# Optimization experiments

Hardware: AMD Instinct MI355X
Metric: run time of the kernel (lower is better)

## Reference

```python
import jax, jax.numpy as jnp
import numpy as np
import math

B, S, F, H, E = 2, 1024, 512, 2048, 8
EPS = 1e-10

def setup_inputs() -> dict:
    key = jax.random.key(0)
    ks = jax.random.split(key, 6)
    s1 = math.sqrt(1.0 / (F + H))  # complex_xavier_init std for F->H
    s2 = math.sqrt(1.0 / (H + F))  # std for H->F
    return {
        'x_r': jax.random.normal(ks[0], (B, S, F), jnp.float32),
        'x_i': jax.random.normal(ks[1], (B, S, F), jnp.float32),
        'Wr1': jax.random.normal(ks[2], (E, F, H), jnp.float32) * s1,
        'Wi1': jax.random.normal(ks[3], (E, F, H), jnp.float32) * s1,
        'br1': jnp.zeros((E, H), jnp.float32),
        'bi1': jnp.zeros((E, H), jnp.float32),
        'mb': jnp.zeros((E, H), jnp.float32),  # ModReLU bias
        'Wr2': jax.random.normal(ks[4], (E, H, F), jnp.float32) * s2,
        'Wi2': jax.random.normal(ks[5], (E, H, F), jnp.float32) * s2,
        'br2': jnp.zeros((E, F), jnp.float32),
        'bi2': jnp.zeros((E, F), jnp.float32),
    }

def reference(x_r, x_i, Wr1, Wi1, br1, bi1, mb, Wr2, Wi2, br2, bi2):
    n_exp = Wr1.shape[0]
    # --- PhaseRouter: deterministic top-1 routing by mean token phase ---
    phase = jnp.arctan2(x_i, x_r)                      # angle(x), (B,S,F)
    mean_cos = jnp.mean(jnp.cos(phase), axis=-1)
    mean_sin = jnp.mean(jnp.sin(phase), axis=-1)
    token_phase = jnp.arctan2(mean_sin, mean_cos)      # (B,S)
    norm_phase = (token_phase + jnp.pi) / (2 * jnp.pi)
    idx = jnp.clip(jnp.floor(norm_phase * n_exp).astype(jnp.int32), 0, n_exp - 1)
    probs = jax.nn.one_hot(idx, n_exp, dtype=x_r.dtype)  # (B,S,E)
    # --- dense all-expert complex MLP (as in source: every expert on every token) ---
    # layer 1: complex linear F->H, per expert
    h_r = (jnp.einsum('bsf,efh->ebsh', x_r, Wr1) - jnp.einsum('bsf,efh->ebsh', x_i, Wi1)
           + br1[:, None, None, :])
    h_i = (jnp.einsum('bsf,efh->ebsh', x_r, Wi1) + jnp.einsum('bsf,efh->ebsh', x_i, Wr1)
           + bi1[:, None, None, :])
    # ModReLU: relu(|z|+b) * z/(|z|+eps)
    amp = jnp.sqrt(h_r * h_r + h_i * h_i + EPS)
    scale = jax.nn.relu(amp + mb[:, None, None, :]) / (amp + EPS)
    h_r = scale * h_r
    h_i = scale * h_i
    # layer 2: complex linear H->F, per expert
    y_r = (jnp.einsum('ebsh,ehf->ebsf', h_r, Wr2) - jnp.einsum('ebsh,ehf->ebsf', h_i, Wi2)
           + br2[:, None, None, :])
    y_i = (jnp.einsum('ebsh,ehf->ebsf', h_r, Wi2) + jnp.einsum('ebsh,ehf->ebsf', h_i, Wr2)
           + bi2[:, None, None, :])
    # combine: expert_weight * mask == probs * probs (one-hot, 0/1)
    w = probs * probs                                   # (B,S,E)
    out_r = jnp.einsum('ebsf,bse->bsf', y_r, w)
    out_i = jnp.einsum('ebsf,bse->bsf', y_i, w)
    return jnp.stack([out_r, out_i])                    # (2,B,S,F): real, imag
```

## Files before the change

### kernel.cpp

```cpp
#include <hip/hip_runtime.h>
#include <hip/hip_bf16.h>

#define TOKENS 2048
#define FDIM 512
#define HDIM 2048
#define NEXP 8
#define PI_F 3.14159265358979323846f

typedef __attribute__((ext_vector_type(8))) short bf16x8;
typedef __attribute__((ext_vector_type(4))) float f32x4;

__device__ __forceinline__ unsigned short f2bf(float f) {
  unsigned int u = __float_as_uint(f);
  unsigned int r = (u + 0x7fffu + ((u >> 16) & 1u)) >> 16;
  return (unsigned short)r;
}

__device__ __forceinline__ void gload16(const void* g, void* l) {
  __builtin_amdgcn_global_load_lds(
      (const __attribute__((address_space(1))) unsigned int*)g,
      (__attribute__((address_space(3))) unsigned int*)l, 16, 0, 0);
}

template<int K, int N>
__device__ __forceinline__ void pack_w_body(
    const float* __restrict__ Wr, const float* __restrict__ Wi,
    short* __restrict__ Wp, int b, float (*tr)[33], float (*ti)[33])
{
  int per_e = (K / 32) * (N / 32);
  int e = b / per_e;
  int rem = b % per_e;
  int k0 = (rem / (N / 32)) * 32, n0 = (rem % (N / 32)) * 32;
  int tid = threadIdx.x;
  int row = tid >> 3, c4 = (tid & 7) * 4;
  const float* wr = Wr + ((size_t)e * K + k0) * N + n0;
  const float* wi = Wi + ((size_t)e * K + k0) * N + n0;
  float4 vr = *(const float4*)(wr + (size_t)row * N + c4);
  float4 vi = *(const float4*)(wi + (size_t)row * N + c4);
  *(float4*)&tr[row][c4] = vr;
  *(float4*)&ti[row][c4] = vi;
  __syncthreads();
  int nl = tid >> 3, k4 = (tid & 7) * 4;
  unsigned short pr[4], pi[4];
  #pragma unroll
  for (int j = 0; j < 4; ++j) {
    pr[j] = f2bf(tr[k4 + j][nl]);
    pi[j] = f2bf(ti[k4 + j][nl]);
  }
  size_t b0 = (((size_t)e * 2 + 0) * N + n0 + nl) * K + k0 + k4;
  size_t b1 = (((size_t)e * 2 + 1) * N + n0 + nl) * K + k0 + k4;
  *(int2*)(Wp + b0) = *(const int2*)pr;
  *(int2*)(Wp + b1) = *(const int2*)pi;
}

__global__ __launch_bounds__(256) void route_packw_kernel(
    const float* __restrict__ xr, const float* __restrict__ xi,
    int* __restrict__ idx, int* __restrict__ counts,
    const float* __restrict__ Wr1, const float* __restrict__ Wi1,
    const float* __restrict__ Wr2, const float* __restrict__ Wi2,
    short* __restrict__ W1p, short* __restrict__ W2p)
{
  __shared__ float tr[32][33], ti[32][33];
  int bid = blockIdx.x;
  if (bid < 256) {
    int tid = threadIdx.x;
    int t = bid * 8 + (tid >> 5);
    int l = tid & 31;
    const float* r  = xr + (size_t)t * FDIM;
    const float* im = xi + (size_t)t * FDIM;
    float sc = 0.f, ss = 0.f;
    #pragma unroll
    for (int p = 0; p < 4; ++p) {
      int f = p * 128 + l * 4;
      float4 a4 = *(const float4*)(r + f);
      float4 b4 = *(const float4*)(im + f);
      float av[4] = {a4.x, a4.y, a4.z, a4.w};
      float bv[4] = {b4.x, b4.y, b4.z, b4.w};
      #pragma unroll
      for (int j = 0; j < 4; ++j) {
        float h2 = av[j] * av[j] + bv[j] * bv[j];
        if (h2 > 0.f) {
          float rs = rsqrtf(h2);
          sc += av[j] * rs;
          ss += bv[j] * rs;
        } else {
          sc += 1.f;
        }
      }
    }
    #pragma unroll
    for (int off = 16; off > 0; off >>= 1) {
      sc += __shfl_down(sc, off, 32);
      ss += __shfl_down(ss, off, 32);
    }
    if (l == 0) {
      float phase = atan2f(ss, sc);
      float norm = (phase + PI_F) / (2.f * PI_F);
      int e = (int)floorf(norm * (float)NEXP);
      e = min(max(e, 0), NEXP - 1);
      idx[t] = e;
      atomicAdd(&counts[e], 1);
    }
  } else {
    int b = bid - 256;
    if (b < 8192) pack_w_body<FDIM, HDIM>(Wr1, Wi1, W1p, b, tr, ti);
    else          pack_w_body<HDIM, FDIM>(Wr2, Wi2, W2p, b - 8192, tr, ti);
  }
}

__global__ __launch_bounds__(256) void scatter_kernel(
    const int* __restrict__ idx, const int* __restrict__ counts,
    int* __restrict__ offs, int* __restrict__ perm, int* __restrict__ rexp)
{
  __shared__ int base_e[NEXP];
  __shared__ int tcnt[256][NEXP];
  int tid = threadIdx.x;
  if (tid == 0) {
    int acc = 0;
    for (int e = 0; e < NEXP; ++e) { base_e[e] = acc; offs[e] = acc; acc += counts[e]; }
  }
  int t0 = tid * 8;
  int eo[8];
  int loc[NEXP];
  #pragma unroll
  for (int e = 0; e < NEXP; ++e) loc[e] = 0;
  #pragma unroll
  for (int j = 0; j < 8; ++j) { eo[j] = idx[t0 + j]; loc[eo[j]]++; }
  #pragma unroll
  for (int e = 0; e < NEXP; ++e) tcnt[tid][e] = loc[e];
  __syncthreads();
  if (tid < NEXP) {
    int e = tid, run = 0;
    for (int i = 0; i < 256; ++i) { int v = tcnt[i][e]; tcnt[i][e] = run; run += v; }
  }
  __syncthreads();
  #pragma unroll
  for (int e = 0; e < NEXP; ++e) loc[e] = base_e[e] + tcnt[tid][e];
  #pragma unroll
  for (int j = 0; j < 8; ++j) {
    int e = eo[j];
    int pos = loc[e]++;
    perm[pos] = t0 + j;
    rexp[pos] = e;
  }
}

__global__ __launch_bounds__(256) void pack_x_kernel(
    const float* __restrict__ xr, const float* __restrict__ xi,
    const int* __restrict__ perm,
    short* __restrict__ Ar, short* __restrict__ Ai)
{
  int gid = blockIdx.x * 256 + threadIdx.x;
  int i = gid >> 7;
  int c4 = (gid & 127) * 4;
  int tok = perm[i];
  float4 r = *(const float4*)(xr + (size_t)tok * FDIM + c4);
  float4 m = *(const float4*)(xi + (size_t)tok * FDIM + c4);
  unsigned short orr[4] = { f2bf(r.x), f2bf(r.y), f2bf(r.z), f2bf(r.w) };
  unsigned short oii[4] = { f2bf(m.x), f2bf(m.y), f2bf(m.z), f2bf(m.w) };
  *(int2*)(Ar + (size_t)i * FDIM + c4) = *(const int2*)orr;
  *(int2*)(Ai + (size_t)i * FDIM + c4) = *(const int2*)oii;
}

template<int LDK, int NC, int NX, bool IS_L1>
__global__ __launch_bounds__(256) void gemm_cplx(
    const short* __restrict__ Apr, const short* __restrict__ Api,
    const short* __restrict__ Wp,
    const int* __restrict__ counts, const int* __restrict__ offs,
    const float* __restrict__ bre, const float* __restrict__ bim,
    const float* __restrict__ mb,
    short* __restrict__ Or, short* __restrict__ Oi,
    unsigned int* __restrict__ P)
{
  constexpr int KT = 16;
  int bid = blockIdx.x;
  int virt = (bid & 7) * 256 + (bid >> 3);
  int e = virt >> 8, rem = virt & 255;
  int x = rem % NX;
  int q = rem / NX;
  int y = q & 7, s = q >> 3;
  int cnt = counts[e];
  int row0 = y * 64;
  if (row0 >= cnt) return;
  int base = offs[e];
  int n0c = x * 64;
  int kbase = s * 512;

  __shared__ __align__(16) short As[2][2][64][32];
  __shared__ __align__(16) short Ws[2][2][64][32];

  int tid = threadIdx.x;
  int lane = tid & 63;
  int w = tid >> 6, wm = w >> 1, wn = w & 1;
  int lr = lane & 15, g = lane >> 4;
  int ssw = g ^ ((lr >> 1) & 3);

  int srl = tid >> 2, slt = tid & 3;
  int sc = (slt ^ ((srl >> 1) & 3)) * 16;
  int arow = min(row0 + srl, cnt - 1);
  const char* pAr = (const char*)(Apr + (size_t)(base + arow) * LDK + kbase) + sc;
  const char* pAi = (const char*)(Api + (size_t)(base + arow) * LDK + kbase) + sc;
  const short* We = Wp + (size_t)e * 2 * NC * LDK;
  const char* pW0 = (const char*)(We + (size_t)(n0c + srl) * LDK + kbase) + sc;
  const char* pW1 = (const char*)(We + ((size_t)NC + n0c + srl) * LDK + kbase) + sc;

  auto STAGE = [&](int buf, int t) {
    char* ab = (char*)&As[0][0][0][0] + buf * 8192;
    gload16(pAr + t * 64, ab + tid * 16);
    gload16(pAi + t * 64, ab + 4096 + tid * 16);
    char* wb = (char*)&Ws[0][0][0][0] + buf * 8192;
    gload16(pW0 + t * 64, wb + tid * 16);
    gload16(pW1 + t * 64, wb + 4096 + tid * 16);
  };

  f32x4 accr[2][2], acci[2][2];
  #pragma unroll
  for (int m = 0; m < 2; ++m)
    #pragma unroll
    for (int n = 0; n < 2; ++n) { accr[m][n] = 0.f; acci[m][n] = 0.f; }

  const bf16x8 SGN = {(short)0x8000, (short)0x8000, (short)0x8000, (short)0x8000,
                      (short)0x8000, (short)0x8000, (short)0x8000, (short)0x8000};

  auto COMPUTE = [&](int buf) {
    const short* Ab = &As[0][0][0][0] + buf * 4096;
    const short* Wb = &Ws[0][0][0][0] + buf * 4096;
    bf16x8 ar[2], ai[2], wr[2], wi[2], wni[2];
    #pragma unroll
    for (int m = 0; m < 2; ++m) {
      int off = (wm * 32 + m * 16 + lr) * 32 + ssw * 8;
      ar[m] = *(const bf16x8*)(Ab + off);
      ai[m] = *(const bf16x8*)(Ab + 2048 + off);
    }
    #pragma unroll
    for (int n = 0; n < 2; ++n) {
      int offw = (wn * 32 + n * 16 + lr) * 32 + ssw * 8;
      wr[n] = *(const bf16x8*)(Wb + offw);
      wi[n] = *(const bf16x8*)(Wb + 2048 + offw);
      wni[n] = wi[n] ^ SGN;
    }
    #pragma unroll
    for (int m = 0; m < 2; ++m)
      #pragma unroll
      for (int n = 0; n < 2; ++n) {
        accr[m][n] = __builtin_amdgcn_mfma_f32_16x16x32_bf16(ar[m], wr[n],  accr[m][n], 0, 0, 0);
        accr[m][n] = __builtin_amdgcn_mfma_f32_16x16x32_bf16(ai[m], wni[n], accr[m][n], 0, 0, 0);
        acci[m][n] = __builtin_amdgcn_mfma_f32_16x16x32_bf16(ar[m], wi[n],  acci[m][n], 0, 0, 0);
        acci[m][n] = __builtin_amdgcn_mfma_f32_16x16x32_bf16(ai[m], wr[n],  acci[m][n], 0, 0, 0);
      }
  };

  STAGE(0, 0);
  STAGE(1, 1);
  for (int t = 0; t < KT; ++t) {
    if (t < KT - 1) asm volatile("s_waitcnt vmcnt(4)" ::: "memory");
    else            asm volatile("s_waitcnt vmcnt(0)" ::: "memory");
    __builtin_amdgcn_s_barrier();
    COMPUTE(t & 1);
    __builtin_amdgcn_s_barrier();
    if (t + 2 < KT) STAGE(t & 1, t + 2);
  }

  #pragma unroll
  for (int m = 0; m < 2; ++m) {
    #pragma unroll
    for (int qq = 0; qq < 4; ++qq) {
      int row = row0 + wm * 32 + m * 16 + g * 4 + qq;
      if (row >= cnt) continue;
      #pragma unroll
      for (int n = 0; n < 2; ++n) {
        int c = n0c + wn * 32 + n * 16 + lr;
        if constexpr (IS_L1) {
          float hr = accr[m][n][qq] + bre[e * NC + c];
          float hi = acci[m][n][qq] + bim[e * NC + c];
          float s2 = hr * hr + hi * hi + 1e-10f;
          float rr = __frsqrt_rn(s2);
          float amp = s2 * rr;
          float scl = fmaxf(amp + mb[e * NC + c], 0.f) * rr;
          Or[(size_t)(base + row) * NC + c] = (short)f2bf(hr * scl);
          Oi[(size_t)(base + row) * NC + c] = (short)f2bf(hi * scl);
        } else {
          unsigned pv = (unsigned)f2bf(accr[m][n][qq])
                      | ((unsigned)f2bf(acci[m][n][qq]) << 16);
          P[((size_t)s * TOKENS + base + row) * 512 + c] = pv;
        }
      }
    }
  }
}

__global__ __launch_bounds__(256) void finalize_kernel(
    const unsigned int* __restrict__ P, const float* __restrict__ br2,
    const float* __restrict__ bi2, const int* __restrict__ perm,
    const int* __restrict__ rexp, float* __restrict__ out)
{
  int gid = blockIdx.x * 256 + threadIdx.x;
  int i = gid >> 7;
  int c4 = (gid & 127) * 4;
  float sr[4] = {0.f, 0.f, 0.f, 0.f}, si[4] = {0.f, 0.f, 0.f, 0.f};
  #pragma unroll
  for (int s = 0; s < 4; ++s) {
    uint4 u = *(const uint4*)(P + ((size_t)s * TOKENS + i) * 512 + c4);
    unsigned uv[4] = {u.x, u.y, u.z, u.w};
    #pragma unroll
    for (int j = 0; j < 4; ++j) {
      sr[j] += __uint_as_float(uv[j] << 16);
      si[j] += __uint_as_float(uv[j] & 0xFFFF0000u);
    }
  }
  int e = rexp[i], tok = perm[i];
  float4 br = *(const float4*)(br2 + e * FDIM + c4);
  float4 bi = *(const float4*)(bi2 + e * FDIM + c4);
  float4 vr = {sr[0] + br.x, sr[1] + br.y, sr[2] + br.z, sr[3] + br.w};
  float4 vi = {si[0] + bi.x, si[1] + bi.y, si[2] + bi.z, si[3] + bi.w};
  *(float4*)(out + (size_t)tok * FDIM + c4) = vr;
  *(float4*)(out + (size_t)TOKENS * FDIM + (size_t)tok * FDIM + c4) = vi;
}

extern "C" void kernel_launch(void* const* d_in, const int* in_sizes, int n_in,
                              void* d_out, int out_size, void* d_ws, size_t ws_size,
                              hipStream_t stream)
{
  const float* xr  = (const float*)d_in[0];
  const float* xi  = (const float*)d_in[1];
  const float* Wr1 = (const float*)d_in[2];
  const float* Wi1 = (const float*)d_in[3];
  const float* br1 = (const float*)d_in[4];
  const float* bi1 = (const float*)d_in[5];
  const float* mb  = (const float*)d_in[6];
  const float* Wr2 = (const float*)d_in[7];
  const float* Wi2 = (const float*)d_in[8];
  const float* br2 = (const float*)d_in[9];
  const float* bi2 = (const float*)d_in[10];
  float* out = (float*)d_out;

  char* ws = (char*)d_ws;
  int* counts = (int*)(ws + 0);
  int* offs   = (int*)(ws + 64);
  int* idx    = (int*)(ws + 128);
  int* perm   = (int*)(ws + 8320);
  int* rexp   = (int*)(ws + 16512);

  size_t off = 32768;
  short* A1r = (short*)(ws + off); off += (size_t)TOKENS * FDIM * 2;
  short* A1i = (short*)(ws + off); off += (size_t)TOKENS * FDIM * 2;
  short* A2r = (short*)(ws + off); off += (size_t)TOKENS * HDIM * 2;
  short* A2i = (short*)(ws + off); off += (size_t)TOKENS * HDIM * 2;
  short* W1p = (short*)(ws + off); off += (size_t)NEXP * 2 * HDIM * FDIM * 2;
  short* W2p = (short*)(ws + off); off += (size_t)NEXP * 2 * FDIM * HDIM * 2;
  unsigned int* P = (unsigned int*)(ws + off);

  hipMemsetAsync(counts, 0, 64, stream);
  route_packw_kernel<<<256 + 16384, 256, 0, stream>>>(
      xr, xi, idx, counts, Wr1, Wi1, Wr2, Wi2, W1p, W2p);
  scatter_kernel<<<1, 256, 0, stream>>>(idx, counts, offs, perm, rexp);
  pack_x_kernel<<<TOKENS * 128 / 256, 256, 0, stream>>>(xr, xi, perm, A1r, A1i);

  gemm_cplx<FDIM, HDIM, 32, true><<<2048, 256, 0, stream>>>(
      A1r, A1i, W1p, counts, offs, br1, bi1, mb, A2r, A2i, nullptr);
  gemm_cplx<HDIM, FDIM, 8, false><<<2048, 256, 0, stream>>>(
      A2r, A2i, W2p, counts, offs, nullptr, nullptr, nullptr, nullptr, nullptr, P);

  finalize_kernel<<<TOKENS * 128 / 256, 256, 0, stream>>>(
      P, br2, bi2, perm, rexp, out);
}
```

Before: 123.1 us.

## Widen weight-pack tiles to 64x32 and simplify GEMM double-buffer loop

The weight repacking path now has each block transpose and convert a 64x32 tile instead of 32x32. That halves the number of pack blocks and lets each thread write 16-byte bf16 chunks. The complex GEMM main loop drops the prefetch-two-ahead scheme with explicit vmcnt waits and two barriers. It now uses a single __syncthreads per iteration, then prefetches the next K tile into the other buffer while computing the current one. This cuts barrier overhead and simplifies the schedule, but prefetch depth shrinks from two tiles to one, so global-load latency may be hidden less well.

```diff
diff --git a/kernel.cpp b/kernel.cpp
--- a/kernel.cpp
+++ b/kernel.cpp
@@ -23,34 +23,37 @@
 }
 
 template<int K, int N>
-__device__ __forceinline__ void pack_w_body(
+__device__ __forceinline__ void pack_w_body64(
     const float* __restrict__ Wr, const float* __restrict__ Wi,
     short* __restrict__ Wp, int b, float (*tr)[33], float (*ti)[33])
 {
-  int per_e = (K / 32) * (N / 32);
+  constexpr int NT_ = N / 32;
+  int per_e = (K / 64) * NT_;
   int e = b / per_e;
   int rem = b % per_e;
-  int k0 = (rem / (N / 32)) * 32, n0 = (rem % (N / 32)) * 32;
+  int k0 = (rem / NT_) * 64, n0 = (rem % NT_) * 32;
   int tid = threadIdx.x;
-  int row = tid >> 3, c4 = (tid & 7) * 4;
-  const float* wr = Wr + ((size_t)e * K + k0) * N + n0;
-  const float* wi = Wi + ((size_t)e * K + k0) * N + n0;
-  float4 vr = *(const float4*)(wr + (size_t)row * N + c4);
-  float4 vi = *(const float4*)(wi + (size_t)row * N + c4);
-  *(float4*)&tr[row][c4] = vr;
-  *(float4*)&ti[row][c4] = vi;
+  int row = tid >> 2, c8 = (tid & 3) * 8;
+  const float* wr = Wr + ((size_t)e * K + k0 + row) * N + n0 + c8;
+  const float* wi = Wi + ((size_t)e * K + k0 + row) * N + n0 + c8;
+  float4 a0 = *(const float4*)(wr);
+  float4 a1 = *(const float4*)(wr + 4);
+  float4 b0 = *(const float4*)(wi);
+  float4 b1 = *(const float4*)(wi + 4);
+  *(float4*)&tr[row][c8] = a0;  *(float4*)&tr[row][c8 + 4] = a1;
+  *(float4*)&ti[row][c8] = b0;  *(float4*)&ti[row][c8 + 4] = b1;
   __syncthreads();
-  int nl = tid >> 3, k4 = (tid & 7) * 4;
-  unsigned short pr[4], pi[4];
-  #pragma unroll
-  for (int j = 0; j < 4; ++j) {
-    pr[j] = f2bf(tr[k4 + j][nl]);
-    pi[j] = f2bf(ti[k4 + j][nl]);
-  }
-  size_t b0 = (((size_t)e * 2 + 0) * N + n0 + nl) * K + k0 + k4;
-  size_t b1 = (((size_t)e * 2 + 1) * N + n0 + nl) * K + k0 + k4;
-  *(int2*)(Wp + b0) = *(const int2*)pr;
-  *(int2*)(Wp + b1) = *(const int2*)pi;
+  int nl = tid >> 3, k8 = (tid & 7) * 8;
+  unsigned short pr[8], pi[8];
+  #pragma unroll
+  for (int j = 0; j < 8; ++j) {
+    pr[j] = f2bf(tr[k8 + j][nl]);
+    pi[j] = f2bf(ti[k8 + j][nl]);
+  }
+  size_t d0 = (((size_t)e * 2 + 0) * N + n0 + nl) * K + k0 + k8;
+  size_t d1 = (((size_t)e * 2 + 1) * N + n0 + nl) * K + k0 + k8;
+  *(int4*)(Wp + d0) = *(const int4*)pr;
+  *(int4*)(Wp + d1) = *(const int4*)pi;
 }
 
 __global__ __launch_bounds__(256) void route_packw_kernel(
@@ -60,7 +63,7 @@
     const float* __restrict__ Wr2, const float* __restrict__ Wi2,
     short* __restrict__ W1p, short* __restrict__ W2p)
 {
-  __shared__ float tr[32][33], ti[32][33];
+  __shared__ float tr[64][33], ti[64][33];
   int bid = blockIdx.x;
   if (bid < 256) {
     int tid = threadIdx.x;
@@ -103,8 +106,8 @@
     }
   } else {
     int b = bid - 256;
-    if (b < 8192) pack_w_body<FDIM, HDIM>(Wr1, Wi1, W1p, b, tr, ti);
-    else          pack_w_body<HDIM, FDIM>(Wr2, Wi2, W2p, b - 8192, tr, ti);
+    if (b < 4096) pack_w_body64<FDIM, HDIM>(Wr1, Wi1, W1p, b, tr, ti);
+    else          pack_w_body64<HDIM, FDIM>(Wr2, Wi2, W2p, b - 4096, tr, ti);
   }
 }
 
@@ -251,14 +254,12 @@
   };
 
   STAGE(0, 0);
-  STAGE(1, 1);
+  int cur = 0;
   for (int t = 0; t < KT; ++t) {
-    if (t < KT - 1) asm volatile("s_waitcnt vmcnt(4)" ::: "memory");
-    else            asm volatile("s_waitcnt vmcnt(0)" ::: "memory");
-    __builtin_amdgcn_s_barrier();
-    COMPUTE(t & 1);
-    __builtin_amdgcn_s_barrier();
-    if (t + 2 < KT) STAGE(t & 1, t + 2);
+    __syncthreads();
+    if (t + 1 < KT) STAGE(cur ^ 1, t + 1);
+    COMPUTE(cur);
+    cur ^= 1;
   }
 
   #pragma unroll
@@ -351,7 +352,7 @@
   unsigned int* P = (unsigned int*)(ws + off);
 
   hipMemsetAsync(counts, 0, 64, stream);
-  route_packw_kernel<<<256 + 16384, 256, 0, stream>>>(
+  route_packw_kernel<<<256 + 8192, 256, 0, stream>>>(
       xr, xi, idx, counts, Wr1, Wi1, Wr2, Wi2, W1p, W2p);
   scatter_kernel<<<1, 256, 0, stream>>>(idx, counts, offs, perm, rexp);
   pack_x_kernel<<<TOKENS * 128 / 256, 256, 0, stream>>>(xr, xi, perm, A1r, A1i);
```

Result: slower. 128.2 us (+4.2%).
